# Kernel optimization log

Measured on AMD Instinct MI355X. Metric: run time of the kernel, lower is better.

The kernel has to match this reference:

```python
import jax, jax.numpy as jnp
import numpy as np

B, S, D, H = 2, 2048, 1024, 16
HEAD_DIM = D // H  # 64


def setup_inputs() -> dict:
    key = jax.random.key(0)
    ks = jax.random.split(key, 7)
    x = jax.random.normal(ks[0], (B, S, D), dtype=jnp.float32)
    W_q = jax.random.normal(ks[1], (D, D), dtype=jnp.float32) * 0.02
    W_k = jax.random.normal(ks[2], (D, D), dtype=jnp.float32) * 0.02
    W_v = jax.random.normal(ks[3], (D, D), dtype=jnp.float32) * 0.02
    W_o = jax.random.normal(ks[4], (D, D), dtype=jnp.float32) * 0.02 / np.sqrt(2 * 12)
    b_o = jnp.zeros((D,), dtype=jnp.float32)
    # Ragged prefix attention_mask: per-row valid lengths in [S/2, S];
    # row 0 forced to full length so max_valid_len == S statically (jit-safe).
    lengths = jax.random.randint(ks[5], (B,), S // 2, S + 1)
    lengths = lengths.at[0].set(S)
    attention_mask = (jnp.arange(S)[None, :] < lengths[:, None]).astype(jnp.float32)
    return {"x": x, "attention_mask": attention_mask, "W_q": W_q, "W_k": W_k,
            "W_v": W_v, "W_o": W_o, "b_o": b_o}


def reference(x, attention_mask, W_q, W_k, W_v, W_o, b_o):
    b, s, d = x.shape
    h, hd = H, HEAD_DIM
    # QKV projections (no bias, qkv_bias=False)
    q = (x @ W_q.T).reshape(b, s, h, hd).transpose(0, 2, 1, 3)  # [b,h,s,hd]
    # Masking keys/values at invalid (padded) positions; for prefix masks this
    # is exactly the module's per-batch packing loop (max_valid_len == s).
    m = attention_mask[:, None, :, None]  # [b,1,s,1]
    k = ((x @ W_k.T).reshape(b, s, h, hd).transpose(0, 2, 1, 3)) * m
    v = ((x @ W_v.T).reshape(b, s, h, hd).transpose(0, 2, 1, 3)) * m
    # Naive causal attention, same op order as the torch module:
    # mask with -inf first, then scale by 1/sqrt(head_dim), then softmax.
    causal = jnp.triu(jnp.ones((s, s), dtype=bool), 1)  # True above diagonal
    scores = jnp.einsum('bhqd,bhkd->bhqk', q, k)
    scores = jnp.where(causal[None, None], -jnp.inf, scores)
    att = jax.nn.softmax(scores / jnp.sqrt(jnp.float32(hd)), axis=-1)
    ctx = jnp.einsum('bhqk,bhkd->bhqd', att, v)  # [b,h,s,hd]
    ctx = ctx.transpose(0, 2, 1, 3).reshape(b, s, d)
    # Output projection (dropout is inference no-op)
    return ctx @ W_o.T + b_o
```

## Files before the change

kernel.cpp:

```cpp
#include <hip/hip_runtime.h>

#define B_  2
#define S_  2048
#define D_  1024
#define H_  16
#define HD_ 64
#define N3_ 3072
#define M_  4096

typedef _Float16 f16;
typedef _Float16 f16x2 __attribute__((ext_vector_type(2)));
typedef _Float16 f16x4 __attribute__((ext_vector_type(4)));
typedef _Float16 f16x8 __attribute__((ext_vector_type(8)));
typedef float    f32x4 __attribute__((ext_vector_type(4)));

__device__ __forceinline__ void async16(const f16* g, f16* l) {
  __builtin_amdgcn_global_load_lds(
      (const __attribute__((address_space(1))) unsigned int*)g,
      (__attribute__((address_space(3))) unsigned int*)l, 16, 0, 0);
}

__device__ __forceinline__ f16x2 pkrtz(float a, float b) {
  return __builtin_bit_cast(f16x2, __builtin_amdgcn_cvt_pkrtz(a, b));
}

__global__ __launch_bounds__(256)
void cvt_all(const float* __restrict__ x,
             const float* __restrict__ Wq, const float* __restrict__ Wk,
             const float* __restrict__ Wv, const float* __restrict__ Wo,
             f16* __restrict__ xb, f16* __restrict__ wdst, float qscale) {
  const int i = blockIdx.x * 256 + threadIdx.x;
  const int XN4 = M_ * D_ / 4;
  const int WN4 = D_ * D_ / 4;
  const float* src;
  f16* dst;
  float scale = 1.0f;
  int j;
  if (i < XN4) {
    src = x; dst = xb; j = i;
  } else {
    int k = i - XN4;
    int m = k >> 18;
    j = k & (WN4 - 1);
    src = (m == 0) ? Wq : (m == 1) ? Wk : (m == 2) ? Wv : Wo;
    if (m == 0) scale = qscale;
    dst = wdst + (size_t)m * D_ * D_;
  }
  float4 v = ((const float4*)src)[j];
  f16x4 o = { (f16)(v.x * scale), (f16)(v.y * scale),
              (f16)(v.z * scale), (f16)(v.w * scale) };
  ((f16x4*)dst)[j] = o;
}

__global__ __launch_bounds__(256)
void gemm_qkv(const f16* __restrict__ A, const f16* __restrict__ Bw,
              f16* __restrict__ Cq, f16* __restrict__ vtout,
              const float* __restrict__ mask) {
  __shared__ f16 As[2][128 * 64];
  __shared__ f16 Bs[2][128 * 64];

  const int tid  = threadIdx.x;
  const int lane = tid & 63;
  const int w    = tid >> 6;
  const int lcol = lane & 15;
  const int quad = lane >> 4;
  const int lx   = lcol & 7;
  const int wave_m = w >> 1, wave_n = w & 1;

  const int m0 = blockIdx.y * 128;
  const int n0 = blockIdx.x * 128;

  const int rr  = lane >> 3;
  const int gch = (lane & 7) ^ rr;

  const f16* gA[4];
  const f16* gB[4];
  int soff[4];
#pragma unroll
  for (int i = 0; i < 4; i++) {
    int seg = i * 4 + w;
    int row = seg * 8 + rr;
    gA[i] = A  + (size_t)(m0 + row) * D_ + gch * 8;
    gB[i] = Bw + (size_t)(n0 + row) * D_ + gch * 8;
    soff[i] = seg * 512;
  }

  auto stage = [&](int k0, int buf) {
#pragma unroll
    for (int i = 0; i < 4; i++) async16(gA[i] + k0, As[buf] + soff[i]);
#pragma unroll
    for (int i = 0; i < 4; i++) async16(gB[i] + k0, Bs[buf] + soff[i]);
  };

  int offA[4], offB[4];
#pragma unroll
  for (int i = 0; i < 4; i++) {
    offA[i] = (wave_m * 64 + i * 16 + lcol) * 64;
    offB[i] = (wave_n * 64 + i * 16 + lcol) * 64;
  }

  const f32x4 zero = {0.f, 0.f, 0.f, 0.f};
  f32x4 acc[4][4];
#pragma unroll
  for (int i = 0; i < 4; i++)
#pragma unroll
    for (int j = 0; j < 4; j++) acc[i][j] = zero;

  const int niter = D_ >> 6;
  stage(0, 0);
  for (int it = 0; it < niter; it++) {
    __syncthreads();
    if (it + 1 < niter) stage((it + 1) << 6, (it + 1) & 1);

    const f16* Ab = As[it & 1];
    const f16* Bb = Bs[it & 1];
#pragma unroll
    for (int ks = 0; ks < 2; ks++) {
      const int co = ((quad + 4 * ks) ^ lx) * 8;
      f16x8 af[4], bf[4];
#pragma unroll
      for (int i = 0; i < 4; i++) af[i] = *(const f16x8*)(Ab + offA[i] + co);
#pragma unroll
      for (int i = 0; i < 4; i++) bf[i] = *(const f16x8*)(Bb + offB[i] + co);
#pragma unroll
      for (int mi = 0; mi < 4; mi++)
#pragma unroll
        for (int ni = 0; ni < 4; ni++)
          acc[mi][ni] = __builtin_amdgcn_mfma_f32_16x16x32_f16(
              af[mi], bf[ni], acc[mi][ni], 0, 0, 0);
    }
  }

  if (n0 >= 2 * D_) {
#pragma unroll
    for (int mi = 0; mi < 4; mi++) {
      const int mgb = m0 + wave_m * 64 + mi * 16 + quad * 4;
      const int b = mgb >> 11, s = mgb & (S_ - 1);
      const float mk0 = mask[mgb], mk1 = mask[mgb + 1];
      const float mk2 = mask[mgb + 2], mk3 = mask[mgb + 3];
#pragma unroll
      for (int ni = 0; ni < 4; ni++) {
        const int vcol = n0 - 2 * D_ + wave_n * 64 + ni * 16 + lcol;
        f16x4 v = { (f16)(acc[mi][ni][0] * mk0), (f16)(acc[mi][ni][1] * mk1),
                    (f16)(acc[mi][ni][2] * mk2), (f16)(acc[mi][ni][3] * mk3) };
        *(f16x4*)(vtout +
                  ((size_t)(b * 16 + (vcol >> 6)) * 64 + (vcol & 63)) * S_ + s) = v;
      }
    }
  } else {
    const bool kmask = (n0 >= D_);
#pragma unroll
    for (int mi = 0; mi < 4; mi++) {
#pragma unroll
      for (int r = 0; r < 4; r++) {
        int mg = m0 + wave_m * 64 + mi * 16 + quad * 4 + r;
        float mk = kmask ? mask[mg] : 1.0f;
#pragma unroll
        for (int ni = 0; ni < 4; ni++) {
          int ng = n0 + wave_n * 64 + ni * 16 + lcol;
          Cq[(size_t)mg * N3_ + ng] = (f16)(acc[mi][ni][r] * mk);
        }
      }
    }
  }
}

__global__ __launch_bounds__(256)
void gemm_proj(const f16* __restrict__ A, const f16* __restrict__ Bw,
               float* __restrict__ Cf, const float* __restrict__ bias) {
  __shared__ f16 As[2][64 * 64];
  __shared__ f16 Bs[2][128 * 64];

  const int tid  = threadIdx.x;
  const int lane = tid & 63;
  const int w    = tid >> 6;
  const int lcol = lane & 15;
  const int quad = lane >> 4;
  const int lx   = lcol & 7;
  const int wave_m = w >> 1, wave_n = w & 1;

  const int m0 = blockIdx.y * 64;
  const int n0 = blockIdx.x * 128;

  const int rr  = lane >> 3;
  const int gch = (lane & 7) ^ rr;

  const f16* gA[2];
  const f16* gB[4];
  int sA[2], sB[4];
#pragma unroll
  for (int i = 0; i < 2; i++) {
    int seg = 2 * w + i;
    gA[i] = A + (size_t)(m0 + seg * 8 + rr) * D_ + gch * 8;
    sA[i] = seg * 512;
  }
#pragma unroll
  for (int i = 0; i < 4; i++) {
    int seg = i * 4 + w;
    gB[i] = Bw + (size_t)(n0 + seg * 8 + rr) * D_ + gch * 8;
    sB[i] = seg * 512;
  }

  auto stage = [&](int k0, int buf) {
#pragma unroll
    for (int i = 0; i < 2; i++) async16(gA[i] + k0, As[buf] + sA[i]);
#pragma unroll
    for (int i = 0; i < 4; i++) async16(gB[i] + k0, Bs[buf] + sB[i]);
  };

  int offA[2], offB[4];
#pragma unroll
  for (int i = 0; i < 2; i++) offA[i] = (wave_m * 32 + i * 16 + lcol) * 64;
#pragma unroll
  for (int i = 0; i < 4; i++) offB[i] = (wave_n * 64 + i * 16 + lcol) * 64;

  const f32x4 zero = {0.f, 0.f, 0.f, 0.f};
  f32x4 acc[2][4];
#pragma unroll
  for (int i = 0; i < 2; i++)
#pragma unroll
    for (int j = 0; j < 4; j++) acc[i][j] = zero;

  const int niter = D_ >> 6;
  stage(0, 0);
  for (int it = 0; it < niter; it++) {
    __syncthreads();
    if (it + 1 < niter) stage((it + 1) << 6, (it + 1) & 1);

    const f16* Ab = As[it & 1];
    const f16* Bb = Bs[it & 1];
#pragma unroll
    for (int ks = 0; ks < 2; ks++) {
      const int co = ((quad + 4 * ks) ^ lx) * 8;
      f16x8 af[2], bf[4];
#pragma unroll
      for (int i = 0; i < 2; i++) af[i] = *(const f16x8*)(Ab + offA[i] + co);
#pragma unroll
      for (int i = 0; i < 4; i++) bf[i] = *(const f16x8*)(Bb + offB[i] + co);
#pragma unroll
      for (int mi = 0; mi < 2; mi++)
#pragma unroll
        for (int ni = 0; ni < 4; ni++)
          acc[mi][ni] = __builtin_amdgcn_mfma_f32_16x16x32_f16(
              af[mi], bf[ni], acc[mi][ni], 0, 0, 0);
    }
  }

#pragma unroll
  for (int mi = 0; mi < 2; mi++) {
#pragma unroll
    for (int r = 0; r < 4; r++) {
      int mg = m0 + wave_m * 32 + mi * 16 + quad * 4 + r;
#pragma unroll
      for (int ni = 0; ni < 4; ni++) {
        int ng = n0 + wave_n * 64 + ni * 16 + lcol;
        Cf[(size_t)mg * D_ + ng] = acc[mi][ni][r] + bias[ng];
      }
    }
  }
}

__global__ __launch_bounds__(256)
void flash_attn6(const f16* __restrict__ qkv, const f16* __restrict__ vt,
                 f16* __restrict__ ctx) {
  __shared__ f16 Ks[64 * 64];
  __shared__ f16 Vs[64 * 64];

  const int tid  = threadIdx.x;
  const int lane = tid & 63;
  const int w    = tid >> 6;
  const int lcol = lane & 15;
  const int quad = lane >> 4;
  const int lx   = lcol & 7;

  const int id   = blockIdx.x;
  const int bh   = (id & 7) + 8 * ((id >> 3) & 3);
  const int pair = id >> 5;
  const int b    = bh >> 4, h = bh & 15;
  const int qtA  = 31 - pair;
  const int qtB  = pair;

  const int rsub = lane >> 3;
  const int gch  = (lane & 7) ^ rsub;
  const int krow0 = w * 8 + rsub;
  const int krow1 = 32 + w * 8 + rsub;
  const f16* Kg = qkv + (size_t)b * S_ * N3_ + D_ + h * HD_;
  const f16* Vg = vt + (size_t)bh * HD_ * S_;
  f16* ldsK0 = Ks + (w * 8) * 64;
  f16* ldsK1 = Ks + (32 + w * 8) * 64;
  f16* ldsV0 = Vs + (w * 8) * 64;
  f16* ldsV1 = Vs + (32 + w * 8) * 64;

  const f32x4 zero = {0.f, 0.f, 0.f, 0.f};

  const int qrowA = qtA * 64 + w * 16 + lcol;
  const int qrowB = qtB * 64 + w * 16 + lcol;
  const f16* QpA = qkv + (size_t)(b * S_ + qrowA) * N3_ + h * HD_;
  const f16* QpB = qkv + (size_t)(b * S_ + qrowB) * N3_ + h * HD_;
  const f16x8 qbA0 = *(const f16x8*)(QpA + quad * 8);
  const f16x8 qbA1 = *(const f16x8*)(QpA + 32 + quad * 8);
  const f16x8 qbB0 = *(const f16x8*)(QpB + quad * 8);
  const f16x8 qbB1 = *(const f16x8*)(QpB + 32 + quad * 8);

  f32x4 oA[4], oB[4];
  f32x4 sumA = zero, sumB = zero;
#pragma unroll
  for (int i = 0; i < 4; i++) { oA[i] = zero; oB[i] = zero; }

  const f16 one_h = (f16)(lcol == 0 ? 1.0f : 0.0f);
  const f16x4 af_ones = { one_h, one_h, one_h, one_h };

  auto mask_diag = [&](f32x4* sc) {
#pragma unroll
    for (int ct = 0; ct < 4; ct++) {
      int koff = ct * 16 + quad * 4;
      int qoff = w * 16 + lcol;
#pragma unroll
      for (int r = 0; r < 4; r++)
        if (koff + r > qoff) sc[ct][r] = -1e30f;
    }
  };
  auto softmax_tiles = [&](f32x4* sc, f16x4* pf, f32x4& sum) {
#pragma unroll
    for (int ct = 0; ct < 4; ct++) {
      f16x2 lo = pkrtz(exp2f(sc[ct][0]), exp2f(sc[ct][1]));
      f16x2 hi = pkrtz(exp2f(sc[ct][2]), exp2f(sc[ct][3]));
      f16x4 p = { lo[0], lo[1], hi[0], hi[1] };
      pf[ct] = p;
      sum = __builtin_amdgcn_mfma_f32_16x16x16f16(af_ones, p, sum, 0, 0, 0);
    }
  };

  for (int kt = 0; kt <= qtA; kt++) {
    const int kbase = kt * 64;
    __syncthreads();
    async16(Kg + (size_t)(kbase + krow0) * N3_ + gch * 8, ldsK0);
    async16(Kg + (size_t)(kbase + krow1) * N3_ + gch * 8, ldsK1);
    async16(Vg + (size_t)krow0 * S_ + kbase + gch * 8, ldsV0);
    async16(Vg + (size_t)krow1 * S_ + kbase + gch * 8, ldsV1);
    __syncthreads();

    const bool doB = (kt <= qtB);

    f16x8 kf0[4], kf1[4];
    f32x4 scA[4], scB[4];
#pragma unroll
    for (int ct = 0; ct < 4; ct++) {
      const f16* kr = Ks + (ct * 16 + lcol) * 64;
      kf0[ct] = *(const f16x8*)(kr + ((quad    ) ^ lx) * 8);
      kf1[ct] = *(const f16x8*)(kr + ((quad + 4) ^ lx) * 8);
      f32x4 z = zero;
      z = __builtin_amdgcn_mfma_f32_16x16x32_f16(kf0[ct], qbA0, z, 0, 0, 0);
      z = __builtin_amdgcn_mfma_f32_16x16x32_f16(kf1[ct], qbA1, z, 0, 0, 0);
      scA[ct] = z;
    }
    if (doB) {
#pragma unroll
      for (int ct = 0; ct < 4; ct++) {
        f32x4 z = zero;
        z = __builtin_amdgcn_mfma_f32_16x16x32_f16(kf0[ct], qbB0, z, 0, 0, 0);
        z = __builtin_amdgcn_mfma_f32_16x16x32_f16(kf1[ct], qbB1, z, 0, 0, 0);
        scB[ct] = z;
      }
    }

    if (kt == qtA) mask_diag(scA);
    if (doB && kt == qtB) mask_diag(scB);

    f16x4 pfA[4], pfB[4];
    softmax_tiles(scA, pfA, sumA);
    if (doB) softmax_tiles(scB, pfB, sumB);

#pragma unroll
    for (int ht = 0; ht < 4; ht++) {
      const f16* vr = Vs + (ht * 16 + lcol) * 64 + (quad & 1) * 4;
      f16x4 vf[4];
#pragma unroll
      for (int ct = 0; ct < 4; ct++)
        vf[ct] = *(const f16x4*)(vr + (((2 * ct + (quad >> 1)) ^ lx) * 8));
#pragma unroll
      for (int ct = 0; ct < 4; ct++)
        oA[ht] = __builtin_amdgcn_mfma_f32_16x16x16f16(vf[ct], pfA[ct], oA[ht], 0, 0, 0);
      if (doB) {
#pragma unroll
        for (int ct = 0; ct < 4; ct++)
          oB[ht] = __builtin_amdgcn_mfma_f32_16x16x16f16(vf[ct], pfB[ct], oB[ht], 0, 0, 0);
      }
    }
  }

  const float lpA = __shfl(sumA[0], lcol);
  const float lpB = __shfl(sumB[0], lcol);
  const float invA = 1.f / lpA;
  const float invB = 1.f / lpB;
  f16* cpA = ctx + (size_t)(b * S_ + qrowA) * D_ + h * HD_ + quad * 4;
  f16* cpB = ctx + (size_t)(b * S_ + qrowB) * D_ + h * HD_ + quad * 4;
#pragma unroll
  for (int ht = 0; ht < 4; ht++) {
    f16x4 ovA = { (f16)(oA[ht][0] * invA), (f16)(oA[ht][1] * invA),
                  (f16)(oA[ht][2] * invA), (f16)(oA[ht][3] * invA) };
    *(f16x4*)(cpA + ht * 16) = ovA;
    f16x4 ovB = { (f16)(oB[ht][0] * invB), (f16)(oB[ht][1] * invB),
                  (f16)(oB[ht][2] * invB), (f16)(oB[ht][3] * invB) };
    *(f16x4*)(cpB + ht * 16) = ovB;
  }
}

extern "C" void kernel_launch(void* const* d_in, const int* in_sizes, int n_in,
                              void* d_out, int out_size, void* d_ws, size_t ws_size,
                              hipStream_t stream) {
  (void)in_sizes; (void)n_in; (void)out_size; (void)ws_size;
  const float* x  = (const float*)d_in[0];
  const float* am = (const float*)d_in[1];
  const float* Wq = (const float*)d_in[2];
  const float* Wk = (const float*)d_in[3];
  const float* Wv = (const float*)d_in[4];
  const float* Wo = (const float*)d_in[5];
  const float* bo = (const float*)d_in[6];
  float* out = (float*)d_out;

  f16* ws   = (f16*)d_ws;
  f16* wqkv = ws;
  f16* wo16 = wqkv + (size_t)3 * D_ * D_;
  f16* xb   = wo16 + (size_t)D_ * D_;
  f16* qkvb = xb + (size_t)M_ * D_;
  f16* vtb  = qkvb + (size_t)M_ * N3_;
  f16* ctxb = vtb + (size_t)M_ * D_;

  const float qscale = 0.125f * 1.4426950408889634f;

  cvt_all<<<dim3((M_ * D_ + 4 * D_ * D_) / 1024), 256, 0, stream>>>(
      x, Wq, Wk, Wv, Wo, xb, wqkv, qscale);

  gemm_qkv<<<dim3(N3_ / 128, M_ / 128), 256, 0, stream>>>(
      xb, wqkv, qkvb, vtb, am);
  flash_attn6<<<dim3(512), 256, 0, stream>>>(qkvb, vtb, ctxb);
  gemm_proj<<<dim3(D_ / 128, M_ / 64), 256, 0, stream>>>(
      ctxb, wo16, out, bo);
}
```

Baseline: 200.0 us.

## Use 128-key tiles in flash attention and single-buffer the GEMM staging

The attention kernel now loads 128-key K and V tiles per iteration instead of 64. It uses a wider swizzled V layout and fuses scoring, diagonal masking, exp and PV accumulation per 16-key column tile. This halves the number of barrier-separated load phases and lowers register pressure from holding whole score tiles. Both GEMMs drop their double-buffered LDS staging for a single buffer with load-then-barrier, which cuts LDS use but stops global loads from overlapping with MFMA work.

```diff
diff --git a/kernel.cpp b/kernel.cpp
--- a/kernel.cpp
+++ b/kernel.cpp
@@ -56,8 +56,8 @@
 void gemm_qkv(const f16* __restrict__ A, const f16* __restrict__ Bw,
               f16* __restrict__ Cq, f16* __restrict__ vtout,
               const float* __restrict__ mask) {
-  __shared__ f16 As[2][128 * 64];
-  __shared__ f16 Bs[2][128 * 64];
+  __shared__ f16 As[128 * 64];
+  __shared__ f16 Bs[128 * 64];
 
   const int tid  = threadIdx.x;
   const int lane = tid & 63;
@@ -75,22 +75,17 @@
 
   const f16* gA[4];
   const f16* gB[4];
-  int soff[4];
+  f16* lA[4];
+  f16* lB[4];
 #pragma unroll
   for (int i = 0; i < 4; i++) {
     int seg = i * 4 + w;
     int row = seg * 8 + rr;
     gA[i] = A  + (size_t)(m0 + row) * D_ + gch * 8;
     gB[i] = Bw + (size_t)(n0 + row) * D_ + gch * 8;
-    soff[i] = seg * 512;
-  }
-
-  auto stage = [&](int k0, int buf) {
-#pragma unroll
-    for (int i = 0; i < 4; i++) async16(gA[i] + k0, As[buf] + soff[i]);
-#pragma unroll
-    for (int i = 0; i < 4; i++) async16(gB[i] + k0, Bs[buf] + soff[i]);
-  };
+    lA[i] = As + seg * 512;
+    lB[i] = Bs + seg * 512;
+  }
 
   int offA[4], offB[4];
 #pragma unroll
@@ -106,22 +101,22 @@
 #pragma unroll
     for (int j = 0; j < 4; j++) acc[i][j] = zero;
 
-  const int niter = D_ >> 6;
-  stage(0, 0);
-  for (int it = 0; it < niter; it++) {
-    __syncthreads();
-    if (it + 1 < niter) stage((it + 1) << 6, (it + 1) & 1);
-
-    const f16* Ab = As[it & 1];
-    const f16* Bb = Bs[it & 1];
+  for (int k0 = 0; k0 < D_; k0 += 64) {
+    __syncthreads();
+#pragma unroll
+    for (int i = 0; i < 4; i++) async16(gA[i] + k0, lA[i]);
+#pragma unroll
+    for (int i = 0; i < 4; i++) async16(gB[i] + k0, lB[i]);
+    __syncthreads();
+
 #pragma unroll
     for (int ks = 0; ks < 2; ks++) {
       const int co = ((quad + 4 * ks) ^ lx) * 8;
       f16x8 af[4], bf[4];
 #pragma unroll
-      for (int i = 0; i < 4; i++) af[i] = *(const f16x8*)(Ab + offA[i] + co);
-#pragma unroll
-      for (int i = 0; i < 4; i++) bf[i] = *(const f16x8*)(Bb + offB[i] + co);
+      for (int i = 0; i < 4; i++) af[i] = *(const f16x8*)(As + offA[i] + co);
+#pragma unroll
+      for (int i = 0; i < 4; i++) bf[i] = *(const f16x8*)(Bs + offB[i] + co);
 #pragma unroll
       for (int mi = 0; mi < 4; mi++)
 #pragma unroll
@@ -168,8 +163,8 @@
 __global__ __launch_bounds__(256)
 void gemm_proj(const f16* __restrict__ A, const f16* __restrict__ Bw,
                float* __restrict__ Cf, const float* __restrict__ bias) {
-  __shared__ f16 As[2][64 * 64];
-  __shared__ f16 Bs[2][128 * 64];
+  __shared__ f16 As[64 * 64];
+  __shared__ f16 Bs[128 * 64];
 
   const int tid  = threadIdx.x;
   const int lane = tid & 63;
@@ -187,26 +182,20 @@
 
   const f16* gA[2];
   const f16* gB[4];
-  int sA[2], sB[4];
+  f16* lA[2];
+  f16* lB[4];
 #pragma unroll
   for (int i = 0; i < 2; i++) {
     int seg = 2 * w + i;
     gA[i] = A + (size_t)(m0 + seg * 8 + rr) * D_ + gch * 8;
-    sA[i] = seg * 512;
+    lA[i] = As + seg * 512;
   }
 #pragma unroll
   for (int i = 0; i < 4; i++) {
     int seg = i * 4 + w;
     gB[i] = Bw + (size_t)(n0 + seg * 8 + rr) * D_ + gch * 8;
-    sB[i] = seg * 512;
-  }
-
-  auto stage = [&](int k0, int buf) {
-#pragma unroll
-    for (int i = 0; i < 2; i++) async16(gA[i] + k0, As[buf] + sA[i]);
-#pragma unroll
-    for (int i = 0; i < 4; i++) async16(gB[i] + k0, Bs[buf] + sB[i]);
-  };
+    lB[i] = Bs + seg * 512;
+  }
 
   int offA[2], offB[4];
 #pragma unroll
@@ -221,22 +210,22 @@
 #pragma unroll
     for (int j = 0; j < 4; j++) acc[i][j] = zero;
 
-  const int niter = D_ >> 6;
-  stage(0, 0);
-  for (int it = 0; it < niter; it++) {
-    __syncthreads();
-    if (it + 1 < niter) stage((it + 1) << 6, (it + 1) & 1);
-
-    const f16* Ab = As[it & 1];
-    const f16* Bb = Bs[it & 1];
+  for (int k0 = 0; k0 < D_; k0 += 64) {
+    __syncthreads();
+#pragma unroll
+    for (int i = 0; i < 2; i++) async16(gA[i] + k0, lA[i]);
+#pragma unroll
+    for (int i = 0; i < 4; i++) async16(gB[i] + k0, lB[i]);
+    __syncthreads();
+
 #pragma unroll
     for (int ks = 0; ks < 2; ks++) {
       const int co = ((quad + 4 * ks) ^ lx) * 8;
       f16x8 af[2], bf[4];
 #pragma unroll
-      for (int i = 0; i < 2; i++) af[i] = *(const f16x8*)(Ab + offA[i] + co);
-#pragma unroll
-      for (int i = 0; i < 4; i++) bf[i] = *(const f16x8*)(Bb + offB[i] + co);
+      for (int i = 0; i < 2; i++) af[i] = *(const f16x8*)(As + offA[i] + co);
+#pragma unroll
+      for (int i = 0; i < 4; i++) bf[i] = *(const f16x8*)(Bs + offB[i] + co);
 #pragma unroll
       for (int mi = 0; mi < 2; mi++)
 #pragma unroll
@@ -261,10 +250,10 @@
 }
 
 __global__ __launch_bounds__(256)
-void flash_attn6(const f16* __restrict__ qkv, const f16* __restrict__ vt,
+void flash_attn7(const f16* __restrict__ qkv, const f16* __restrict__ vt,
                  f16* __restrict__ ctx) {
-  __shared__ f16 Ks[64 * 64];
-  __shared__ f16 Vs[64 * 64];
+  __shared__ f16 Ks[128 * 64];
+  __shared__ f16 Vs[64 * 128];
 
   const int tid  = threadIdx.x;
   const int lane = tid & 63;
@@ -279,17 +268,15 @@
   const int b    = bh >> 4, h = bh & 15;
   const int qtA  = 31 - pair;
   const int qtB  = pair;
+  const int ktA  = qtA >> 1;
+  const int ktB  = qtB >> 1;
 
   const int rsub = lane >> 3;
-  const int gch  = (lane & 7) ^ rsub;
-  const int krow0 = w * 8 + rsub;
-  const int krow1 = 32 + w * 8 + rsub;
+  const int gchK = (lane & 7) ^ rsub;
+  const int vsub = lane >> 4;
+  const int gchV = (lane & 15) ^ ((w * 4 + vsub) & 7);
   const f16* Kg = qkv + (size_t)b * S_ * N3_ + D_ + h * HD_;
   const f16* Vg = vt + (size_t)bh * HD_ * S_;
-  f16* ldsK0 = Ks + (w * 8) * 64;
-  f16* ldsK1 = Ks + (32 + w * 8) * 64;
-  f16* ldsV0 = Vs + (w * 8) * 64;
-  f16* ldsV1 = Vs + (32 + w * 8) * 64;
 
   const f32x4 zero = {0.f, 0.f, 0.f, 0.f};
 
@@ -310,81 +297,71 @@
   const f16 one_h = (f16)(lcol == 0 ? 1.0f : 0.0f);
   const f16x4 af_ones = { one_h, one_h, one_h, one_h };
 
-  auto mask_diag = [&](f32x4* sc) {
-#pragma unroll
-    for (int ct = 0; ct < 4; ct++) {
-      int koff = ct * 16 + quad * 4;
-      int qoff = w * 16 + lcol;
-#pragma unroll
-      for (int r = 0; r < 4; r++)
-        if (koff + r > qoff) sc[ct][r] = -1e30f;
-    }
-  };
-  auto softmax_tiles = [&](f32x4* sc, f16x4* pf, f32x4& sum) {
-#pragma unroll
-    for (int ct = 0; ct < 4; ct++) {
-      f16x2 lo = pkrtz(exp2f(sc[ct][0]), exp2f(sc[ct][1]));
-      f16x2 hi = pkrtz(exp2f(sc[ct][2]), exp2f(sc[ct][3]));
-      f16x4 p = { lo[0], lo[1], hi[0], hi[1] };
-      pf[ct] = p;
-      sum = __builtin_amdgcn_mfma_f32_16x16x16f16(af_ones, p, sum, 0, 0, 0);
-    }
-  };
-
-  for (int kt = 0; kt <= qtA; kt++) {
-    const int kbase = kt * 64;
-    __syncthreads();
-    async16(Kg + (size_t)(kbase + krow0) * N3_ + gch * 8, ldsK0);
-    async16(Kg + (size_t)(kbase + krow1) * N3_ + gch * 8, ldsK1);
-    async16(Vg + (size_t)krow0 * S_ + kbase + gch * 8, ldsV0);
-    async16(Vg + (size_t)krow1 * S_ + kbase + gch * 8, ldsV1);
-    __syncthreads();
-
-    const bool doB = (kt <= qtB);
-
-    f16x8 kf0[4], kf1[4];
-    f32x4 scA[4], scB[4];
-#pragma unroll
-    for (int ct = 0; ct < 4; ct++) {
+  for (int kt = 0; kt <= ktA; kt++) {
+    const int kbase = kt * 128;
+    __syncthreads();
+#pragma unroll
+    for (int i = 0; i < 4; i++) {
+      async16(Kg + (size_t)(kbase + 32 * i + w * 8 + rsub) * N3_ + gchK * 8,
+              Ks + (32 * i + w * 8) * 64);
+      async16(Vg + (size_t)(16 * i + w * 4 + vsub) * S_ + kbase + gchV * 8,
+              Vs + (16 * i + w * 4) * 128);
+    }
+    __syncthreads();
+
+    const bool doB = (kt <= ktB);
+    const bool dgA = (kt == ktA);
+    const bool dgB = (kt == ktB);
+
+#pragma unroll
+    for (int ct = 0; ct < 8; ct++) {
       const f16* kr = Ks + (ct * 16 + lcol) * 64;
-      kf0[ct] = *(const f16x8*)(kr + ((quad    ) ^ lx) * 8);
-      kf1[ct] = *(const f16x8*)(kr + ((quad + 4) ^ lx) * 8);
-      f32x4 z = zero;
-      z = __builtin_amdgcn_mfma_f32_16x16x32_f16(kf0[ct], qbA0, z, 0, 0, 0);
-      z = __builtin_amdgcn_mfma_f32_16x16x32_f16(kf1[ct], qbA1, z, 0, 0, 0);
-      scA[ct] = z;
-    }
-    if (doB) {
-#pragma unroll
-      for (int ct = 0; ct < 4; ct++) {
-        f32x4 z = zero;
-        z = __builtin_amdgcn_mfma_f32_16x16x32_f16(kf0[ct], qbB0, z, 0, 0, 0);
-        z = __builtin_amdgcn_mfma_f32_16x16x32_f16(kf1[ct], qbB1, z, 0, 0, 0);
-        scB[ct] = z;
-      }
-    }
-
-    if (kt == qtA) mask_diag(scA);
-    if (doB && kt == qtB) mask_diag(scB);
-
-    f16x4 pfA[4], pfB[4];
-    softmax_tiles(scA, pfA, sumA);
-    if (doB) softmax_tiles(scB, pfB, sumB);
-
-#pragma unroll
-    for (int ht = 0; ht < 4; ht++) {
-      const f16* vr = Vs + (ht * 16 + lcol) * 64 + (quad & 1) * 4;
-      f16x4 vf[4];
-#pragma unroll
-      for (int ct = 0; ct < 4; ct++)
-        vf[ct] = *(const f16x4*)(vr + (((2 * ct + (quad >> 1)) ^ lx) * 8));
-#pragma unroll
-      for (int ct = 0; ct < 4; ct++)
-        oA[ht] = __builtin_amdgcn_mfma_f32_16x16x16f16(vf[ct], pfA[ct], oA[ht], 0, 0, 0);
+      f16x8 k0 = *(const f16x8*)(kr + ((quad    ) ^ lx) * 8);
+      f16x8 k1 = *(const f16x8*)(kr + ((quad + 4) ^ lx) * 8);
+
+      f32x4 scA = zero;
+      scA = __builtin_amdgcn_mfma_f32_16x16x32_f16(k0, qbA0, scA, 0, 0, 0);
+      scA = __builtin_amdgcn_mfma_f32_16x16x32_f16(k1, qbA1, scA, 0, 0, 0);
+      if (dgA) {
+        const int kg = kbase + ct * 16 + quad * 4;
+#pragma unroll
+        for (int r = 0; r < 4; r++)
+          if (kg + r > qrowA - qtA * 64 + qtA * 64) {}
+#pragma unroll
+        for (int r = 0; r < 4; r++)
+          if (kg + r > qrowA) scA[r] = -1e30f;
+      }
+      f16x2 la = pkrtz(exp2f(scA[0]), exp2f(scA[1]));
+      f16x2 ha = pkrtz(exp2f(scA[2]), exp2f(scA[3]));
+      f16x4 pA = { la[0], la[1], ha[0], ha[1] };
+      sumA = __builtin_amdgcn_mfma_f32_16x16x16f16(af_ones, pA, sumA, 0, 0, 0);
+
+      f16x4 pB;
       if (doB) {
-#pragma unroll
-        for (int ct = 0; ct < 4; ct++)
-          oB[ht] = __builtin_amdgcn_mfma_f32_16x16x16f16(vf[ct], pfB[ct], oB[ht], 0, 0, 0);
+        f32x4 scB = zero;
+        scB = __builtin_amdgcn_mfma_f32_16x16x32_f16(k0, qbB0, scB, 0, 0, 0);
+        scB = __builtin_amdgcn_mfma_f32_16x16x32_f16(k1, qbB1, scB, 0, 0, 0);
+        if (dgB) {
+          const int kg = kbase + ct * 16 + quad * 4;
+#pragma unroll
+          for (int r = 0; r < 4; r++)
+            if (kg + r > qrowB) scB[r] = -1e30f;
+        }
+        f16x2 lb = pkrtz(exp2f(scB[0]), exp2f(scB[1]));
+        f16x2 hb = pkrtz(exp2f(scB[2]), exp2f(scB[3]));
+        f16x4 p = { lb[0], lb[1], hb[0], hb[1] };
+        pB = p;
+        sumB = __builtin_amdgcn_mfma_f32_16x16x16f16(af_ones, pB, sumB, 0, 0, 0);
+      }
+
+#pragma unroll
+      for (int ht = 0; ht < 4; ht++) {
+        const f16* vr = Vs + (ht * 16 + lcol) * 128;
+        f16x4 vf = *(const f16x4*)(vr + (((2 * ct + (quad >> 1)) ^ lx) * 8) +
+                                   (quad & 1) * 4);
+        oA[ht] = __builtin_amdgcn_mfma_f32_16x16x16f16(vf, pA, oA[ht], 0, 0, 0);
+        if (doB)
+          oB[ht] = __builtin_amdgcn_mfma_f32_16x16x16f16(vf, pB, oB[ht], 0, 0, 0);
       }
     }
   }
@@ -434,7 +411,7 @@
 
   gemm_qkv<<<dim3(N3_ / 128, M_ / 128), 256, 0, stream>>>(
       xb, wqkv, qkvb, vtb, am);
-  flash_attn6<<<dim3(512), 256, 0, stream>>>(qkvb, vtb, ctxb);
+  flash_attn7<<<dim3(512), 256, 0, stream>>>(qkvb, vtb, ctxb);
   gemm_proj<<<dim3(D_ / 128, M_ / 64), 256, 0, stream>>>(
       ctxb, wo16, out, bo);
 }
```

After: 205.5 us. 2.7% more time.
